# Kernel tuning notes

Hardware: AMD Instinct MI355X
Metric: run time of the kernel (lower is better)

The kernel has to match this reference:

```python
import jax, jax.numpy as jnp
import numpy as np

B, S, D, H = 4, 2048, 2048, 16
HD = D // H  # head_dim = 128


def setup_inputs() -> dict:
    key = jax.random.key(0)
    ks = jax.random.split(key, 9)
    s = 1.0 / np.sqrt(D)
    return {
        "x": jax.random.normal(ks[0], (B, S, D), dtype=jnp.float32),
        "wq": jax.random.normal(ks[1], (D, D), dtype=jnp.float32) * s,
        "bq": jnp.zeros((D,), dtype=jnp.float32),
        "wk": jax.random.normal(ks[2], (D, D), dtype=jnp.float32) * s,
        "bk": jnp.zeros((D,), dtype=jnp.float32),
        "wv": jax.random.normal(ks[3], (D, D), dtype=jnp.float32) * s,
        "bv": jnp.zeros((D,), dtype=jnp.float32),
        "wo": jax.random.normal(ks[4], (D, D), dtype=jnp.float32) * s,
        "bo": jnp.zeros((D,), dtype=jnp.float32),
    }


def reference(x, wq, bq, wk, bk, wv, bv, wo, bo):
    scale = HD ** -0.5
    # projections: [B,S,D] -> [B,S,H,HD] -> [B,H,S,HD]
    def split_heads(t):
        return t.reshape(B, S, H, HD).transpose(0, 2, 1, 3)
    q = split_heads(x @ wq + bq)
    k = split_heads(x @ wk + bk)
    v = split_heads(x @ wv + bv)
    scores = jnp.einsum('bhqd,bhkd->bhqk', q, k) * scale  # [B,H,S,S]
    attn = jax.nn.softmax(scores, axis=-1)
    out = jnp.einsum('bhqk,bhkd->bhqd', attn, v)  # [B,H,S,HD]
    out = out.transpose(0, 2, 1, 3).reshape(B, S, D)
    return out @ wo + bo
```

## Files before the change

### kernel.cpp

```cpp
#include <hip/hip_runtime.h>
#include <hip/hip_bf16.h>


typedef __attribute__((ext_vector_type(8))) short short8;
typedef __attribute__((ext_vector_type(4))) short short4v;
typedef __attribute__((ext_vector_type(4))) float floatx4;
typedef unsigned int u32;

#define DEV __device__ __forceinline__

DEV short f2bf(float f) {
    __hip_bfloat16 h = __float2bfloat16(f);
    return *reinterpret_cast<short*>(&h);
}

DEV void load_lds16(const __hip_bfloat16* g, short* l) {
    __builtin_amdgcn_global_load_lds(
        (const __attribute__((address_space(1))) void*)g,
        (__attribute__((address_space(3))) void*)l, 16, 0, 0);
}

DEV u32 cvt_pk_bf16(float lo, float hi) {
    u32 r;
    asm("v_cvt_pk_bf16_f32 %0, %1, %2" : "=v"(r) : "v"(lo), "v"(hi));
    return r;
}

__global__ void cast_x_kernel(const float* __restrict__ in,
                              __hip_bfloat16* __restrict__ out, int n8) {
    int i = blockIdx.x * 256 + threadIdx.x;
    if (i >= n8) return;
    const float4* p = reinterpret_cast<const float4*>(in) + (size_t)i * 2;
    float4 a = p[0], b = p[1];
    short8 r;
    r[0] = f2bf(a.x); r[1] = f2bf(a.y); r[2] = f2bf(a.z); r[3] = f2bf(a.w);
    r[4] = f2bf(b.x); r[5] = f2bf(b.y); r[6] = f2bf(b.z); r[7] = f2bf(b.w);
    *reinterpret_cast<short8*>(reinterpret_cast<short*>(out) + (size_t)i * 8) = r;
}

__global__ void transpose_cast_kernel(const float* __restrict__ wq,
                                      const float* __restrict__ wk,
                                      const float* __restrict__ wv,
                                      const float* __restrict__ wo,
                                      short* __restrict__ wt) {
    __shared__ float tile[32][33];
    const int z = blockIdx.z;
    const float* src = (z == 0) ? wq : (z == 1) ? wk : (z == 2) ? wv : wo;
    short* dst = wt + (size_t)z * 2048 * 2048;
    const int tx = threadIdx.x, ty = threadIdx.y;
    const int bx = blockIdx.x, by = blockIdx.y;
#pragma unroll
    for (int j = 0; j < 4; ++j)
        tile[ty + j * 8][tx] = src[(size_t)(by * 32 + ty + j * 8) * 2048 + bx * 32 + tx];
    __syncthreads();
#pragma unroll
    for (int j = 0; j < 4; ++j) {
        int r = ty + j * 8;
        dst[(size_t)(bx * 32 + r) * 2048 + by * 32 + tx] = f2bf(tile[tx][r]);
    }
}

template<int MODE>
__launch_bounds__(256, 2)
__global__ void gemm_bt_kernel(const __hip_bfloat16* __restrict__ A,
                               const __hip_bfloat16* __restrict__ Bt,
                               const float* __restrict__ bias0,
                               const float* __restrict__ bias1,
                               const float* __restrict__ bias2,
                               short* __restrict__ qbuf,
                               short* __restrict__ kbuf,
                               short* __restrict__ vtbuf,
                               float* __restrict__ outf) {
    constexpr int K = 2048;
    __shared__ short As[128 * 64];
    __shared__ short Bs[128 * 64];
    const int t = threadIdx.x, lane = t & 63, wid = t >> 6;
    const int lr = lane & 15, lg = lane >> 4;
    const int n0 = blockIdx.x * 128, m0 = blockIdx.y * 128;
    const int wm = (wid & 1) * 64, wn = (wid >> 1) * 64;

    floatx4 acc[4][4];
#pragma unroll
    for (int i = 0; i < 4; ++i)
#pragma unroll
        for (int j = 0; j < 4; ++j) acc[i][j] = (floatx4){0.f, 0.f, 0.f, 0.f};

    for (int kt = 0; kt < K / 64; ++kt) {
        __syncthreads();
#pragma unroll
        for (int i = 0; i < 4; ++i) {
            int fc = i * 256 + t;
            int row = fc >> 3, p = fc & 7;
            int col = (p ^ (row & 7)) << 3;
            load_lds16(A + (size_t)(m0 + row) * K + kt * 64 + col,
                       &As[(i * 256 + wid * 64) * 8]);
        }
#pragma unroll
        for (int i = 0; i < 4; ++i) {
            int fc = i * 256 + t;
            int row = fc >> 3, p = fc & 7;
            int col = (p ^ (row & 7)) << 3;
            load_lds16(Bt + (size_t)(n0 + row) * K + kt * 64 + col,
                       &Bs[(i * 256 + wid * 64) * 8]);
        }
        __syncthreads();
#pragma unroll
        for (int kk = 0; kk < 2; ++kk) {
            short8 af[4], bfr[4];
#pragma unroll
            for (int mi = 0; mi < 4; ++mi) {
                int row = wm + mi * 16 + lr;
                int c = lg + kk * 4;
                af[mi] = *(const short8*)&As[row * 64 + ((c ^ (row & 7)) << 3)];
            }
#pragma unroll
            for (int ni = 0; ni < 4; ++ni) {
                int row = wn + ni * 16 + lr;
                int c = lg + kk * 4;
                bfr[ni] = *(const short8*)&Bs[row * 64 + ((c ^ (row & 7)) << 3)];
            }
#pragma unroll
            for (int mi = 0; mi < 4; ++mi)
#pragma unroll
                for (int ni = 0; ni < 4; ++ni)
                    acc[mi][ni] = __builtin_amdgcn_mfma_f32_16x16x32_bf16(
                        af[mi], bfr[ni], acc[mi][ni], 0, 0, 0);
        }
    }

#pragma unroll
    for (int ni = 0; ni < 4; ++ni) {
        int n = n0 + wn + ni * 16 + lr;
        if (MODE == 0) {
            int which = n >> 11, d = n & 2047, h = d >> 7, hd = d & 127;
            const float* bias = (which == 0) ? bias0 : (which == 1) ? bias1 : bias2;
            float bval = bias[d];
            short* buf = (which == 0) ? qbuf : (which == 1) ? kbuf : vtbuf;
#pragma unroll
            for (int mi = 0; mi < 4; ++mi) {
                int m = m0 + wm + mi * 16 + lg * 4;
                int b = m >> 11, s = m & 2047;
                int bh = b * 16 + h;
#pragma unroll
                for (int r = 0; r < 4; ++r) {
                    float v = acc[mi][ni][r] + bval;
                    if (which == 0) v *= 0.08838834764831845f;
                    if (which < 2)
                        buf[((size_t)bh * 2048 + s + r) * 128 + hd] = f2bf(v);
                    else
                        buf[((size_t)bh * 128 + hd) * 2048 + s + r] = f2bf(v);
                }
            }
        } else {
            float bval = bias0[n];
#pragma unroll
            for (int mi = 0; mi < 4; ++mi) {
                int m = m0 + wm + mi * 16 + lg * 4;
#pragma unroll
                for (int r = 0; r < 4; ++r)
                    outf[(size_t)(m + r) * 2048 + n] = acc[mi][ni][r] + bval;
            }
        }
    }
}

__launch_bounds__(256, 2)
__global__ void attn_kernel(const __hip_bfloat16* __restrict__ qb,
                            const __hip_bfloat16* __restrict__ kb,
                            const __hip_bfloat16* __restrict__ vtb,
                            short* __restrict__ ob) {
    __shared__ short Ks[2][64 * 128];
    __shared__ short Vts[2][128 * 64];
    __shared__ short Pt[4][32 * 64];

    const int t = threadIdx.x, lane = t & 63, w = t >> 6;
    const int lr = lane & 15, lg = lane >> 4;

    int id = blockIdx.y * 16 + blockIdx.x;
    int xcd = id & 7, slot = id >> 3;
    int bh = xcd * 8 + (slot >> 4);
    int qblk = slot & 15;
    const int b = bh >> 4, h = bh & 15;
    const int q0 = qblk * 128;

    const __hip_bfloat16* qB = qb + (size_t)bh * 2048 * 128;
    const __hip_bfloat16* kB = kb + (size_t)bh * 2048 * 128;
    const __hip_bfloat16* vB = vtb + (size_t)bh * 128 * 2048;

    short8 aq[2][4];
#pragma unroll
    for (int mi = 0; mi < 2; ++mi) {
        int row = q0 + w * 32 + mi * 16 + lr;
#pragma unroll
        for (int kk = 0; kk < 4; ++kk)
            aq[mi][kk] = *(const short8*)(qB + (size_t)row * 128 + lg * 8 + kk * 32);
    }

    floatx4 o[2][8];
    float mv[2], lv[2];
#pragma unroll
    for (int mi = 0; mi < 2; ++mi) {
#pragma unroll
        for (int n = 0; n < 8; ++n) o[mi][n] = (floatx4){0.f, 0.f, 0.f, 0.f};
        mv[mi] = -1e30f; lv[mi] = 0.f;
    }

    auto STAGE = [&](int d, int kv) {
#pragma unroll
        for (int i = 0; i < 4; ++i) {
            int fc = i * 256 + t, row = fc >> 4, p = fc & 15;
            load_lds16(kB + (size_t)(kv * 64 + row) * 128 + ((p ^ (row & 15)) << 3),
                       &Ks[d][(i * 256 + w * 64) * 8]);
        }
#pragma unroll
        for (int i = 0; i < 4; ++i) {
            int fc = i * 256 + t, row = fc >> 3, p = fc & 7;
            load_lds16(vB + (size_t)row * 2048 + kv * 64 + ((p ^ (row & 7)) << 3),
                       &Vts[d][(i * 256 + w * 64) * 8]);
        }
    };

    STAGE(0, 0);
    asm volatile("s_waitcnt vmcnt(0)" ::: "memory");
    __builtin_amdgcn_s_barrier();

    int cur = 0;
    for (int kv = 0; kv < 32; ++kv) {
        if (kv < 31) STAGE(cur ^ 1, kv + 1);

        floatx4 sfr[2][4];
#pragma unroll
        for (int mi = 0; mi < 2; ++mi)
#pragma unroll
            for (int tt = 0; tt < 4; ++tt) sfr[mi][tt] = (floatx4){0.f, 0.f, 0.f, 0.f};
        __builtin_amdgcn_s_setprio(1);
#pragma unroll
        for (int tt = 0; tt < 4; ++tt)
#pragma unroll
            for (int kk = 0; kk < 4; ++kk) {
                int row = tt * 16 + lr;
                int c = lg + kk * 4;
                short8 bk = *(const short8*)&Ks[cur][row * 128 + ((c ^ (row & 15)) << 3)];
                sfr[0][tt] = __builtin_amdgcn_mfma_f32_16x16x32_bf16(bk, aq[0][kk], sfr[0][tt], 0, 0, 0);
                sfr[1][tt] = __builtin_amdgcn_mfma_f32_16x16x32_bf16(bk, aq[1][kk], sfr[1][tt], 0, 0, 0);
            }
        __builtin_amdgcn_s_setprio(0);

#pragma unroll
        for (int mi = 0; mi < 2; ++mi) {
            float pm = sfr[mi][0][0];
#pragma unroll
            for (int tt = 0; tt < 4; ++tt)
#pragma unroll
                for (int r = 0; r < 4; ++r) pm = fmaxf(pm, sfr[mi][tt][r]);
            pm = fmaxf(pm, __shfl_xor(pm, 16));
            pm = fmaxf(pm, __shfl_xor(pm, 32));
            if (!__all(pm - mv[mi] <= 8.f)) {
                float mn = fmaxf(mv[mi], pm);
                float alpha = __expf(mv[mi] - mn);
                mv[mi] = mn;
                lv[mi] *= alpha;
#pragma unroll
                for (int n = 0; n < 8; ++n) o[mi][n] *= alpha;
            }
            float m = mv[mi], ls = 0.f;
            u32 pk[8];
#pragma unroll
            for (int tt = 0; tt < 4; ++tt) {
                float p0 = __expf(sfr[mi][tt][0] - m);
                float p1 = __expf(sfr[mi][tt][1] - m);
                float p2 = __expf(sfr[mi][tt][2] - m);
                float p3 = __expf(sfr[mi][tt][3] - m);
                ls += (p0 + p1) + (p2 + p3);
                pk[tt * 2] = cvt_pk_bf16(p0, p1);
                pk[tt * 2 + 1] = cvt_pk_bf16(p2, p3);
            }
            ls += __shfl_xor(ls, 16);
            ls += __shfl_xor(ls, 32);
            lv[mi] += ls;
#pragma unroll
            for (int tt = 0; tt < 4; ++tt) {
                int hgran = tt * 2 + (lg >> 1);
                int idx = (mi * 16 + lr) * 64 + ((hgran ^ (lr & 7)) * 8) + (lg & 1) * 4;
                *(uint2*)&Pt[w][idx] = make_uint2(pk[tt * 2], pk[tt * 2 + 1]);
            }
        }

        short8 pa[2][2];
#pragma unroll
        for (int mi = 0; mi < 2; ++mi)
#pragma unroll
            for (int kk = 0; kk < 2; ++kk) {
                int hgran = kk * 4 + lg;
                int idx = (mi * 16 + lr) * 64 + ((hgran ^ (lr & 7)) * 8);
                pa[mi][kk] = *(const short8*)&Pt[w][idx];
            }
        __builtin_amdgcn_s_setprio(1);
#pragma unroll
        for (int n = 0; n < 8; ++n)
#pragma unroll
            for (int kk = 0; kk < 2; ++kk) {
                int vrow = n * 16 + lr;
                int c = lg + kk * 4;
                short8 bv = *(const short8*)&Vts[cur][vrow * 64 + ((c ^ (vrow & 7)) << 3)];
                o[0][n] = __builtin_amdgcn_mfma_f32_16x16x32_bf16(bv, pa[0][kk], o[0][n], 0, 0, 0);
                o[1][n] = __builtin_amdgcn_mfma_f32_16x16x32_bf16(bv, pa[1][kk], o[1][n], 0, 0, 0);
            }
        __builtin_amdgcn_s_setprio(0);

        asm volatile("s_waitcnt vmcnt(0)" ::: "memory");
        __builtin_amdgcn_s_barrier();
        cur ^= 1;
    }

#pragma unroll
    for (int mi = 0; mi < 2; ++mi) {
        float inv = 1.f / lv[mi];
        int s = q0 + w * 32 + mi * 16 + lr;
        size_t base = ((size_t)b * 2048 + s) * 2048 + h * 128;
#pragma unroll
        for (int n = 0; n < 8; ++n) {
            short4v vv;
#pragma unroll
            for (int r = 0; r < 4; ++r) vv[r] = f2bf(o[mi][n][r] * inv);
            *(short4v*)&ob[base + n * 16 + lg * 4] = vv;
        }
    }
}

extern "C" void kernel_launch(void* const* d_in, const int* in_sizes, int n_in,
                              void* d_out, int out_size, void* d_ws, size_t ws_size,
                              hipStream_t stream) {
    (void)in_sizes; (void)n_in; (void)out_size; (void)ws_size;
    const float* x  = (const float*)d_in[0];
    const float* wq = (const float*)d_in[1];
    const float* bq = (const float*)d_in[2];
    const float* wk = (const float*)d_in[3];
    const float* bk = (const float*)d_in[4];
    const float* wv = (const float*)d_in[5];
    const float* bv = (const float*)d_in[6];
    const float* wo = (const float*)d_in[7];
    const float* bo = (const float*)d_in[8];
    float* out = (float*)d_out;

    char* ws = (char*)d_ws;
    const size_t SZ = (size_t)33554432;
    __hip_bfloat16* xbf = (__hip_bfloat16*)(ws);
    short* wt    = (short*)(ws + SZ);
    short* qbuf  = (short*)(ws + 2 * SZ);
    short* kbuf  = (short*)(ws + 3 * SZ);
    short* vtbuf = (short*)(ws + 4 * SZ);
    short* obuf  = (short*)(ws);

    cast_x_kernel<<<8192, 256, 0, stream>>>(x, xbf, 2097152);
    transpose_cast_kernel<<<dim3(64, 64, 4), dim3(32, 8), 0, stream>>>(wq, wk, wv, wo, wt);
    gemm_bt_kernel<0><<<dim3(48, 64), 256, 0, stream>>>(
        xbf, (const __hip_bfloat16*)wt, bq, bk, bv, qbuf, kbuf, vtbuf, nullptr);
    attn_kernel<<<dim3(16, 64), 256, 0, stream>>>(
        (const __hip_bfloat16*)qbuf, (const __hip_bfloat16*)kbuf,
        (const __hip_bfloat16*)vtbuf, obuf);
    gemm_bt_kernel<1><<<dim3(16, 64), 256, 0, stream>>>(
        (const __hip_bfloat16*)obuf, (const __hip_bfloat16*)(wt + (size_t)6144 * 2048),
        bo, nullptr, nullptr, nullptr, nullptr, nullptr, out);
}
```

Before: 672.7 us.

## Replace projection GEMMs with 256x256 tile, 8-wave, double-buffered pipelined kernel

Replaces the 128x128 single-buffered GEMM used for the QKV and output projections with a 256x256-tile kernel of 512 threads. It double-buffers LDS in quarter-tile pieces, interleaves global-to-LDS loads with MFMA phases using manual waitcnt and barriers, raises MFMA priority, and swizzles workgroup order across XCDs. The goal is to hide memory latency behind compute and raise operand reuse per tile. In exchange it uses more LDS and registers, runs one block per CU, and the output GEMM launches only 256 workgroups, which may leave CUs idle.

```diff
diff --git a/kernel.cpp b/kernel.cpp
--- a/kernel.cpp
+++ b/kernel.cpp
@@ -61,8 +61,8 @@
 }
 
 template<int MODE>
-__launch_bounds__(256, 2)
-__global__ void gemm_bt_kernel(const __hip_bfloat16* __restrict__ A,
+__launch_bounds__(512, 1)
+__global__ void gemm256_kernel(const __hip_bfloat16* __restrict__ A,
                                const __hip_bfloat16* __restrict__ Bt,
                                const float* __restrict__ bias0,
                                const float* __restrict__ bias1,
@@ -72,96 +72,163 @@
                                short* __restrict__ vtbuf,
                                float* __restrict__ outf) {
     constexpr int K = 2048;
-    __shared__ short As[128 * 64];
-    __shared__ short Bs[128 * 64];
+    constexpr int KT = 32;
+    __shared__ short As[2][2][128 * 64];
+    __shared__ short Bs[2][2][128 * 64];
+
     const int t = threadIdx.x, lane = t & 63, wid = t >> 6;
     const int lr = lane & 15, lg = lane >> 4;
-    const int n0 = blockIdx.x * 128, m0 = blockIdx.y * 128;
-    const int wm = (wid & 1) * 64, wn = (wid >> 1) * 64;
-
-    floatx4 acc[4][4];
-#pragma unroll
-    for (int i = 0; i < 4; ++i)
+    const int wm = wid >> 2, wn = wid & 3;
+
+    int nwg = gridDim.x * gridDim.y;
+    int orig = blockIdx.y * gridDim.x + blockIdx.x;
+    int swz = (orig & 7) * (nwg >> 3) + (orig >> 3);
+    int bx = swz % gridDim.x, by = swz / gridDim.x;
+    const int n0 = bx * 256, m0 = by * 256;
+
+    const __hip_bfloat16* Ab = A + (size_t)m0 * K;
+    const __hip_bfloat16* Bb = Bt + (size_t)n0 * K;
+
+    auto stageA = [&](int s, int kt, int h) {
+#pragma unroll
+        for (int i = 0; i < 2; ++i) {
+            int flat = i * 512 + t;
+            int row = flat >> 3, p = flat & 7;
+            int col = (p ^ (row & 7)) << 3;
+            load_lds16(Ab + (size_t)(h * 128 + row) * K + kt * 64 + col,
+                       &As[s][h][(i * 512 + wid * 64) * 8]);
+        }
+    };
+    auto stageB = [&](int s, int kt, int h) {
+#pragma unroll
+        for (int i = 0; i < 2; ++i) {
+            int flat = i * 512 + t;
+            int row = flat >> 3, p = flat & 7;
+            int col = (p ^ (row & 7)) << 3;
+            load_lds16(Bb + (size_t)(h * 128 + row) * K + kt * 64 + col,
+                       &Bs[s][h][(i * 512 + wid * 64) * 8]);
+        }
+    };
+    auto ldsA = [&](int s, int qm, short8 (&dst)[4][2]) {
+#pragma unroll
+        for (int mi = 0; mi < 4; ++mi)
+#pragma unroll
+            for (int kk = 0; kk < 2; ++kk) {
+                int row = wm * 64 + mi * 16 + lr;
+                int c = lg + kk * 4;
+                dst[mi][kk] = *(const short8*)&As[s][qm][row * 64 + ((c ^ (row & 7)) << 3)];
+            }
+    };
+    auto ldsB = [&](int s, int qn, short8 (&dst)[2][2]) {
+#pragma unroll
+        for (int ni = 0; ni < 2; ++ni)
+#pragma unroll
+            for (int kk = 0; kk < 2; ++kk) {
+                int row = wn * 32 + ni * 16 + lr;
+                int c = lg + kk * 4;
+                dst[ni][kk] = *(const short8*)&Bs[s][qn][row * 64 + ((c ^ (row & 7)) << 3)];
+            }
+    };
+
+    floatx4 acc[8][4];
+#pragma unroll
+    for (int i = 0; i < 8; ++i)
 #pragma unroll
         for (int j = 0; j < 4; ++j) acc[i][j] = (floatx4){0.f, 0.f, 0.f, 0.f};
 
-    for (int kt = 0; kt < K / 64; ++kt) {
-        __syncthreads();
-#pragma unroll
-        for (int i = 0; i < 4; ++i) {
-            int fc = i * 256 + t;
-            int row = fc >> 3, p = fc & 7;
-            int col = (p ^ (row & 7)) << 3;
-            load_lds16(A + (size_t)(m0 + row) * K + kt * 64 + col,
-                       &As[(i * 256 + wid * 64) * 8]);
-        }
-#pragma unroll
-        for (int i = 0; i < 4; ++i) {
-            int fc = i * 256 + t;
-            int row = fc >> 3, p = fc & 7;
-            int col = (p ^ (row & 7)) << 3;
-            load_lds16(Bt + (size_t)(n0 + row) * K + kt * 64 + col,
-                       &Bs[(i * 256 + wid * 64) * 8]);
-        }
-        __syncthreads();
-#pragma unroll
-        for (int kk = 0; kk < 2; ++kk) {
-            short8 af[4], bfr[4];
-#pragma unroll
-            for (int mi = 0; mi < 4; ++mi) {
-                int row = wm + mi * 16 + lr;
-                int c = lg + kk * 4;
-                af[mi] = *(const short8*)&As[row * 64 + ((c ^ (row & 7)) << 3)];
-            }
-#pragma unroll
-            for (int ni = 0; ni < 4; ++ni) {
-                int row = wn + ni * 16 + lr;
-                int c = lg + kk * 4;
-                bfr[ni] = *(const short8*)&Bs[row * 64 + ((c ^ (row & 7)) << 3)];
-            }
-#pragma unroll
-            for (int mi = 0; mi < 4; ++mi)
-#pragma unroll
-                for (int ni = 0; ni < 4; ++ni)
-                    acc[mi][ni] = __builtin_amdgcn_mfma_f32_16x16x32_bf16(
-                        af[mi], bfr[ni], acc[mi][ni], 0, 0, 0);
-        }
-    }
-
-#pragma unroll
-    for (int ni = 0; ni < 4; ++ni) {
-        int n = n0 + wn + ni * 16 + lr;
-        if (MODE == 0) {
-            int which = n >> 11, d = n & 2047, h = d >> 7, hd = d & 127;
-            const float* bias = (which == 0) ? bias0 : (which == 1) ? bias1 : bias2;
-            float bval = bias[d];
-            short* buf = (which == 0) ? qbuf : (which == 1) ? kbuf : vtbuf;
-#pragma unroll
-            for (int mi = 0; mi < 4; ++mi) {
-                int m = m0 + wm + mi * 16 + lg * 4;
-                int b = m >> 11, s = m & 2047;
-                int bh = b * 16 + h;
-#pragma unroll
-                for (int r = 0; r < 4; ++r) {
-                    float v = acc[mi][ni][r] + bval;
-                    if (which == 0) v *= 0.08838834764831845f;
-                    if (which < 2)
-                        buf[((size_t)bh * 2048 + s + r) * 128 + hd] = f2bf(v);
-                    else
-                        buf[((size_t)bh * 128 + hd) * 2048 + s + r] = f2bf(v);
-                }
-            }
-        } else {
-            float bval = bias0[n];
-#pragma unroll
-            for (int mi = 0; mi < 4; ++mi) {
-                int m = m0 + wm + mi * 16 + lg * 4;
-#pragma unroll
-                for (int r = 0; r < 4; ++r)
-                    outf[(size_t)(m + r) * 2048 + n] = acc[mi][ni][r] + bval;
-            }
-        }
-    }
+    short8 af[4][2], b0f[2][2], b1f[2][2];
+
+#define BAR1 __builtin_amdgcn_s_barrier(); \
+             asm volatile("s_waitcnt lgkmcnt(0)" ::: "memory")
+#define BAR2 __builtin_amdgcn_s_barrier()
+#define VM4  asm volatile("s_waitcnt vmcnt(4)" ::: "memory")
+#define MF(MOFF, NOFF, BF)                                                     \
+    __builtin_amdgcn_s_setprio(1);                                             \
+    _Pragma("unroll") for (int mi = 0; mi < 4; ++mi)                           \
+    _Pragma("unroll") for (int ni = 0; ni < 2; ++ni)                           \
+    _Pragma("unroll") for (int kk = 0; kk < 2; ++kk)                           \
+        acc[MOFF + mi][NOFF + ni] = __builtin_amdgcn_mfma_f32_16x16x32_bf16(   \
+            af[mi][kk], BF[ni][kk], acc[MOFF + mi][NOFF + ni], 0, 0, 0);       \
+    __builtin_amdgcn_s_setprio(0)
+
+    stageA(0, 0, 0); stageB(0, 0, 0); stageA(0, 0, 1); stageB(0, 0, 1);
+    stageA(1, 1, 0); stageB(1, 1, 0);
+    VM4;
+    __builtin_amdgcn_s_barrier();
+
+    for (int it = 0; it < KT / 2; ++it) {
+        int k1 = 2 * it + 1;
+        int k2 = (2 * it + 2 < KT) ? 2 * it + 2 : KT - 1;
+        int k3 = (2 * it + 3 < KT) ? 2 * it + 3 : KT - 1;
+        ldsA(0, 0, af); ldsB(0, 0, b0f);
+        stageA(1, k1, 1);
+        BAR1; MF(0, 0, b0f); BAR2;
+        ldsB(0, 1, b1f);
+        stageB(1, k1, 1);
+        BAR1; MF(0, 2, b1f); BAR2;
+        ldsA(0, 1, af);
+        stageA(0, k2, 0);
+        BAR1; MF(4, 2, b1f); BAR2;
+        stageB(0, k2, 0);
+        BAR1; MF(4, 0, b0f); VM4; BAR2;
+        ldsA(1, 0, af); ldsB(1, 0, b0f);
+        stageA(0, k2, 1);
+        BAR1; MF(0, 0, b0f); BAR2;
+        ldsB(1, 1, b1f);
+        stageB(0, k2, 1);
+        BAR1; MF(0, 2, b1f); BAR2;
+        ldsA(1, 1, af);
+        stageA(1, k3, 0);
+        BAR1; MF(4, 2, b1f); BAR2;
+        stageB(1, k3, 0);
+        BAR1; MF(4, 0, b0f); VM4; BAR2;
+    }
+#undef BAR1
+#undef BAR2
+#undef VM4
+#undef MF
+
+#pragma unroll
+    for (int qn = 0; qn < 2; ++qn)
+#pragma unroll
+        for (int ni = 0; ni < 2; ++ni) {
+            int n = n0 + qn * 128 + wn * 32 + ni * 16 + lr;
+            if (MODE == 0) {
+                int which = n >> 11, d = n & 2047, h = d >> 7, hd = d & 127;
+                const float* bias = (which == 0) ? bias0 : (which == 1) ? bias1 : bias2;
+                float bval = bias[d];
+                short* buf = (which == 0) ? qbuf : (which == 1) ? kbuf : vtbuf;
+#pragma unroll
+                for (int qm = 0; qm < 2; ++qm)
+#pragma unroll
+                    for (int mi = 0; mi < 4; ++mi) {
+                        int m = m0 + qm * 128 + wm * 64 + mi * 16 + lg * 4;
+                        int b = m >> 11, s = m & 2047;
+                        int bh = b * 16 + h;
+#pragma unroll
+                        for (int r = 0; r < 4; ++r) {
+                            float v = acc[qm * 4 + mi][qn * 2 + ni][r] + bval;
+                            if (which == 0) v *= 0.08838834764831845f;
+                            if (which < 2)
+                                buf[((size_t)bh * 2048 + s + r) * 128 + hd] = f2bf(v);
+                            else
+                                buf[((size_t)bh * 128 + hd) * 2048 + s + r] = f2bf(v);
+                        }
+                    }
+            } else {
+                float bval = bias0[n];
+#pragma unroll
+                for (int qm = 0; qm < 2; ++qm)
+#pragma unroll
+                    for (int mi = 0; mi < 4; ++mi) {
+                        int m = m0 + qm * 128 + wm * 64 + mi * 16 + lg * 4;
+#pragma unroll
+                        for (int r = 0; r < 4; ++r)
+                            outf[(size_t)(m + r) * 2048 + n] =
+                                acc[qm * 4 + mi][qn * 2 + ni][r] + bval;
+                    }
+            }
+        }
 }
 
 __launch_bounds__(256, 2)
@@ -354,12 +421,12 @@
 
     cast_x_kernel<<<8192, 256, 0, stream>>>(x, xbf, 2097152);
     transpose_cast_kernel<<<dim3(64, 64, 4), dim3(32, 8), 0, stream>>>(wq, wk, wv, wo, wt);
-    gemm_bt_kernel<0><<<dim3(48, 64), 256, 0, stream>>>(
+    gemm256_kernel<0><<<dim3(24, 32), 512, 0, stream>>>(
         xbf, (const __hip_bfloat16*)wt, bq, bk, bv, qbuf, kbuf, vtbuf, nullptr);
     attn_kernel<<<dim3(16, 64), 256, 0, stream>>>(
         (const __hip_bfloat16*)qbuf, (const __hip_bfloat16*)kbuf,
         (const __hip_bfloat16*)vtbuf, obuf);
-    gemm_bt_kernel<1><<<dim3(16, 64), 256, 0, stream>>>(
+    gemm256_kernel<1><<<dim3(8, 32), 512, 0, stream>>>(
         (const __hip_bfloat16*)obuf, (const __hip_bfloat16*)(wt + (size_t)6144 * 2048),
         bo, nullptr, nullptr, nullptr, nullptr, nullptr, out);
 }
```

Result: faster. 640.9 us (-4.7%).
